# Kernel optimization log

Measured on AMD Instinct MI355X. Metric: run time of the kernel, lower is better.

## Reference

```python
import jax, jax.numpy as jnp
import numpy as np

HIDDEN = 300
LN_EPS = 1e-5


def _pair_indices(L, K):
    # row-major (emo, cau) order matches torch cat/reshape in couple_generator
    i = np.arange(L)[:, None]
    j = np.arange(L)[None, :]
    mask = np.abs(j - i) <= K
    emo, cau = np.nonzero(mask)
    return emo.astype(np.int32), cau.astype(np.int32)


def setup_inputs() -> dict:
    key = jax.random.key(0)
    ks = jax.random.split(key, 10)
    B, L, D = 32, 128, HIDDEN
    K = 12
    pos_dim = 50
    inp = {
        "h_e": jax.random.normal(ks[0], (B, L, D), jnp.float32),
        "h_c": jax.random.normal(ks[1], (B, L, D), jnp.float32),
        "h_share": jax.random.normal(ks[2], (B, L, D), jnp.float32),
        "pos_emb": jax.random.normal(ks[3], (2 * K + 1, pos_dim), jnp.float32) * 0.1,
        "W_hid": jax.random.normal(ks[4], (D, 2 * D + pos_dim), jnp.float32) * 0.02,
        "b_hid": jnp.zeros((D,), jnp.float32),
        "ln_g": jnp.ones((D,), jnp.float32),
        "ln_b": jnp.zeros((D,), jnp.float32),
        "W_rel": jax.random.normal(ks[5], (1, D), jnp.float32) * 0.02,
        "b_rel": jnp.zeros((1,), jnp.float32),
        "K": K,
    }
    return inp


def reference(h_e, h_c, h_share, pos_emb, W_hid, b_hid, ln_g, ln_b, W_rel, b_rel, K):
    B, L, D = h_e.shape
    he = h_e + h_share
    hc = h_c + h_share
    emo, cau = _pair_indices(L, int(K))  # static index constants
    rel = (cau - emo).astype(np.float32)  # [n]
    rp = jnp.asarray(cau - emo + int(K), jnp.int32)  # shifted rel pos
    # gather-concat pair features: [B, n, 2D]
    couples = jnp.concatenate([he[:, emo, :], hc[:, cau, :]], axis=-1)
    # Gaussian kernel over relative positions: [n, n]
    rel_j = jnp.asarray(rel)
    kernel = jnp.exp(-jnp.square(rel_j[:, None] - rel_j[None, :]))
    # smooth position embeddings (batch-independent): [n, pos_dim]
    rel_pos_emb = kernel @ pos_emb[rp]
    pair = jnp.concatenate(
        [couples, jnp.broadcast_to(rel_pos_emb[None], (B,) + rel_pos_emb.shape)],
        axis=-1,
    )
    h = jnp.einsum("bnf,df->bnd", pair, W_hid) + b_hid
    mu = jnp.mean(h, axis=-1, keepdims=True)
    var = jnp.mean(jnp.square(h - mu), axis=-1, keepdims=True)
    h = (h - mu) * jax.lax.rsqrt(var + LN_EPS) * ln_g + ln_b
    h = jax.nn.elu(h)  # dropout is identity in eval mode
    out = jnp.einsum("bnd,od->bno", h, W_rel) + b_rel
    return out[..., 0]  # [B, n_couple]
```

## Files before the change

kernel.cpp:

```cpp
#include <hip/hip_runtime.h>
#include <math.h>

#define BB 32
#define LL 128
#define DD 300
#define PD 50
#define KW 12
#define NP 3044
#define FF 650
#define NR 25
#define KP 320
#define MM 4096
#define LN_EPS 1e-5f

typedef __attribute__((ext_vector_type(8))) short short8;
typedef __attribute__((ext_vector_type(4))) float f32x4;
typedef __attribute__((ext_vector_type(4))) int i32x4;

__device__ __forceinline__ unsigned int cvtpk(float lo, float hi) {
    unsigned int r;
    asm("v_cvt_pk_bf16_f32 %0, %1, %2" : "=v"(r) : "v"(lo), "v"(hi));
    return r;
}

__device__ __forceinline__ short8 as_short8(i32x4 v) {
    union { i32x4 i; short8 s; } u; u.i = v; return u.s;
}

__device__ __forceinline__ int row_start(int i) {
    if (i <= 12) return i * 13 + (i * (i - 1)) / 2;
    if (i <= 116) return 222 + 25 * (i - 12);
    int s = i - 116;
    return 2822 + 24 * s - (s * (s - 1)) / 2;
}

struct B8 { float f[8]; };

__global__ __launch_bounds__(512) void fused_kernel(
    const float* __restrict__ h_e, const float* __restrict__ h_c,
    const float* __restrict__ h_share, const float* __restrict__ pos_emb,
    const float* __restrict__ W_hid, const float* __restrict__ b_hid,
    float* __restrict__ E, float* __restrict__ Cc, float* __restrict__ P,
    float* __restrict__ SEp, float* __restrict__ SP)
{
    const int tid = threadIdx.x;

    __shared__ unsigned short Bs[2][160 * 40];

    if (blockIdx.x < NR) {
        __shared__ float sm[PD];
        __shared__ float wsum[8];
        const int r = blockIdx.x;
        if (tid < PD) {
            float acc = 0.f;
            #pragma unroll
            for (int d2 = 0; d2 < NR; d2++) {
                int ad = d2 - KW; if (ad < 0) ad = -ad;
                float cnt = (float)(LL - ad);
                float diff = (float)(r - d2);
                acc += cnt * expf(-diff * diff) * pos_emb[d2 * PD + tid];
            }
            sm[tid] = acc;
        }
        __syncthreads();
        float mine = 0.f;
        if (tid < DD) {
            float a = b_hid[tid];
            const float* w = W_hid + (size_t)tid * FF + 2 * DD;
            #pragma unroll
            for (int k = 0; k < PD; k++) a += sm[k] * w[k];
            P[r * DD + tid] = a;
            mine = a;
        }
        #pragma unroll
        for (int m = 1; m < 64; m <<= 1) mine += __shfl_xor(mine, m, 64);
        if ((tid & 63) == 0) wsum[tid >> 6] = mine;
        __syncthreads();
        if (tid == 0) {
            float s = 0.f;
            #pragma unroll
            for (int w = 0; w < 8; w++) s += wsum[w];
            SP[r] = s;
        }
        return;
    }

    const int gb = blockIdx.x - NR;
    const int sg = (gb & 7) * 32 + (gb >> 3);
    const int m0 = (sg & 63) * 64;
    const int y  = (sg >> 6) & 1;
    const int z  = sg >> 7;
    const int n0 = y * 160;

    const int wid  = tid >> 6;
    const int lane = tid & 63;
    const int wm = wid & 3;
    const int wn = wid >> 1 >> 1;
    const int nn = lane & 15;
    const int q  = lane >> 4;

    const int row = m0 + wm * 16 + nn;
    const float* xr = (z ? h_c : h_e) + (size_t)row * DD;
    const float* sr = h_share + (size_t)row * DD;
    const float* Wsrc = W_hid + z * DD;

    const int n_a = tid >> 2,        c_a = tid & 3;
    const int d_a = n0 + n_a;
    const int n_b = (tid + 512) >> 2;
    const int d_b = n0 + n_b;
    const bool has_b = (tid < 128);

    B8 ra, rb;
    float4 ax0, ax1, as0, as1;

    auto loadB = [&](int k0) {
        const float* pa = Wsrc + (size_t)d_a * FF + k0 + c_a * 8;
        float2 u0 = *(const float2*)(pa);
        float2 u1 = *(const float2*)(pa + 2);
        float2 u2 = *(const float2*)(pa + 4);
        float2 u3 = *(const float2*)(pa + 6);
        ra.f[0] = u0.x; ra.f[1] = u0.y; ra.f[2] = u1.x; ra.f[3] = u1.y;
        ra.f[4] = u2.x; ra.f[5] = u2.y; ra.f[6] = u3.x; ra.f[7] = u3.y;
        if (has_b) {
            if (d_b < DD) {
                const float* pb = Wsrc + (size_t)d_b * FF + k0 + c_a * 8;
                float2 v0 = *(const float2*)(pb);
                float2 v1 = *(const float2*)(pb + 2);
                float2 v2 = *(const float2*)(pb + 4);
                float2 v3 = *(const float2*)(pb + 6);
                rb.f[0] = v0.x; rb.f[1] = v0.y; rb.f[2] = v1.x; rb.f[3] = v1.y;
                rb.f[4] = v2.x; rb.f[5] = v2.y; rb.f[6] = v3.x; rb.f[7] = v3.y;
            } else {
                #pragma unroll
                for (int u = 0; u < 8; u++) rb.f[u] = 0.f;
            }
        }
    };

    auto writeB = [&](int buf) {
        i32x4 w;
        w[0] = cvtpk(ra.f[0], ra.f[1]); w[1] = cvtpk(ra.f[2], ra.f[3]);
        w[2] = cvtpk(ra.f[4], ra.f[5]); w[3] = cvtpk(ra.f[6], ra.f[7]);
        *(i32x4*)&Bs[buf][n_a * 40 + c_a * 8] = w;
        if (has_b) {
            i32x4 v;
            v[0] = cvtpk(rb.f[0], rb.f[1]); v[1] = cvtpk(rb.f[2], rb.f[3]);
            v[2] = cvtpk(rb.f[4], rb.f[5]); v[3] = cvtpk(rb.f[6], rb.f[7]);
            *(i32x4*)&Bs[buf][n_b * 40 + c_a * 8] = v;
        }
    };

    auto loadA = [&](int k0) {
        const int kb = k0 + q * 8;
        if (kb + 7 < DD) {
            ax0 = *(const float4*)&xr[kb];
            ax1 = *(const float4*)&xr[kb + 4];
            as0 = *(const float4*)&sr[kb];
            as1 = *(const float4*)&sr[kb + 4];
        } else {
            float t[8], u[8];
            #pragma unroll
            for (int uu = 0; uu < 8; uu++) {
                int k = kb + uu;
                t[uu] = (k < DD) ? xr[k] : 0.f;
                u[uu] = (k < DD) ? sr[k] : 0.f;
            }
            ax0 = make_float4(t[0], t[1], t[2], t[3]);
            ax1 = make_float4(t[4], t[5], t[6], t[7]);
            as0 = make_float4(u[0], u[1], u[2], u[3]);
            as1 = make_float4(u[4], u[5], u[6], u[7]);
        }
    };

    f32x4 acc[5];
    #pragma unroll
    for (int f = 0; f < 5; f++) acc[f] = (f32x4){0.f, 0.f, 0.f, 0.f};

    loadB(0);
    loadA(0);
    writeB(0);
    __syncthreads();

    #pragma unroll
    for (int k0i = 0; k0i < 10; k0i++) {
        const int cb = k0i & 1;
        const bool more = (k0i < 9);
        const int kn = (k0i + 1) * 32;

        if (more) loadB(kn);

        i32x4 af;
        af[0] = cvtpk(ax0.x + as0.x, ax0.y + as0.y);
        af[1] = cvtpk(ax0.z + as0.z, ax0.w + as0.w);
        af[2] = cvtpk(ax1.x + as1.x, ax1.y + as1.y);
        af[3] = cvtpk(ax1.z + as1.z, ax1.w + as1.w);
        short8 a = as_short8(af);

        if (more) loadA(kn);

        #pragma unroll
        for (int f = 0; f < 5; f++) {
            short8 b = *(const short8*)&Bs[cb][(wn * 80 + f * 16 + nn) * 40 + q * 8];
            acc[f] = __builtin_amdgcn_mfma_f32_16x16x32_bf16(a, b, acc[f], 0, 0, 0);
        }

        if (more) {
            writeB(cb ^ 1);
            __syncthreads();
        }
    }

    const int orow = m0 + wm * 16 + q * 4;
    float rs[4];
    #pragma unroll
    for (int r2 = 0; r2 < 4; r2++) {
        float v = 0.f;
        #pragma unroll
        for (int f = 0; f < 5; f++) v += acc[f][r2];
        #pragma unroll
        for (int m = 1; m < 16; m <<= 1) v += __shfl_xor(v, m, 64);
        rs[r2] = v;
    }
    if (nn == 0) {
        float* slot = SEp + (size_t)(((z * 2 + y) * 2 + wn)) * MM;
        #pragma unroll
        for (int r2 = 0; r2 < 4; r2++) slot[orow + r2] = rs[r2];
    }

    float* O = z ? Cc : E;
    #pragma unroll
    for (int f = 0; f < 5; f++) {
        int col = n0 + wn * 80 + f * 16 + nn;
        if (col < DD) {
            #pragma unroll
            for (int r2 = 0; r2 < 4; r2++)
                O[(size_t)(orow + r2) * DD + col] = acc[f][r2];
        }
    }
}

__global__ __launch_bounds__(320) void pair_kernel(
    const float* __restrict__ E, const float* __restrict__ Cc,
    const float* __restrict__ P, const float* __restrict__ SEp,
    const float* __restrict__ SP, const float* __restrict__ ln_g,
    const float* __restrict__ ln_b, const float* __restrict__ W_rel,
    const float* __restrict__ b_rel, float* __restrict__ out)
{
    const int wid = threadIdx.x >> 6;
    const int lane = threadIdx.x & 63;
    const int slot = (blockIdx.x & 7) * 512 + (blockIdx.x >> 3);
    const int b = slot >> 7;
    const int i = slot & 127;

    const float* e_row = E + (size_t)slot * DD;

    float e[5], g[5], gb[5], wr[5];
    #pragma unroll
    for (int t = 0; t < 5; t++) {
        int d = lane + 64 * t;
        if (d < DD) {
            e[t]  = e_row[d];
            g[t]  = ln_g[d];
            gb[t] = ln_b[d];
            wr[t] = W_rel[d];
        } else {
            e[t] = 0.f; g[t] = 0.f; gb[t] = 0.f; wr[t] = 0.f;
        }
    }
    const float brel = b_rel[0];
    const float SEi = SEp[slot] + SEp[MM + slot] + SEp[2 * MM + slot] + SEp[3 * MM + slot];
    const float* SC = SEp + 4 * MM;

    int jlo = i - KW; if (jlo < 0) jlo = 0;
    int jhi = i + KW; if (jhi > LL - 1) jhi = LL - 1;
    const int base = b * NP + row_start(i);
    const float inv = 1.f / (float)DD;

    for (int j = jlo + wid; j <= jhi; j += 5) {
        const int bj = b * LL + j;
        const int r = j - i + KW;
        const float* c_row = Cc + (size_t)bj * DD;
        const float* p_row = P + r * DD;

        const float sumh = SEi + SC[bj] + SC[MM + bj] + SC[2 * MM + bj]
                         + SC[3 * MM + bj] + SP[r];

        float h[5];
        float ss = 0.f;
        #pragma unroll
        for (int t = 0; t < 5; t++) {
            int d = lane + 64 * t;
            h[t] = 0.f;
            if (d < DD) {
                h[t] = e[t] + c_row[d] + p_row[d];
                ss += h[t] * h[t];
            }
        }
        #pragma unroll
        for (int m = 1; m < 64; m <<= 1) ss += __shfl_xor(ss, m, 64);

        const float mean = sumh * inv;
        float var = ss * inv - mean * mean;
        if (var < 0.f) var = 0.f;
        const float rstd = rsqrtf(var + LN_EPS);

        float acc = 0.f;
        #pragma unroll
        for (int t = 0; t < 5; t++) {
            int d = lane + 64 * t;
            if (d < DD) {
                float yv = (h[t] - mean) * rstd * g[t] + gb[t];
                float el = yv > 0.f ? yv : (__expf(yv) - 1.f);
                acc += el * wr[t];
            }
        }
        #pragma unroll
        for (int m = 1; m < 64; m <<= 1) acc += __shfl_xor(acc, m, 64);

        if (lane == 0) out[base + (j - jlo)] = acc + brel;
    }
}

extern "C" void kernel_launch(void* const* d_in, const int* in_sizes, int n_in,
                              void* d_out, int out_size, void* d_ws, size_t ws_size,
                              hipStream_t stream) {
    const float* h_e     = (const float*)d_in[0];
    const float* h_c     = (const float*)d_in[1];
    const float* h_share = (const float*)d_in[2];
    const float* pos_emb = (const float*)d_in[3];
    const float* W_hid   = (const float*)d_in[4];
    const float* b_hid   = (const float*)d_in[5];
    const float* ln_g    = (const float*)d_in[6];
    const float* ln_b    = (const float*)d_in[7];
    const float* W_rel   = (const float*)d_in[8];
    const float* b_rel   = (const float*)d_in[9];

    float* out = (float*)d_out;

    float* ws  = (float*)d_ws;
    float* E   = ws;
    float* C   = E + (size_t)MM * DD;
    float* P   = C + (size_t)MM * DD;
    float* SEp = P + NR * DD;
    float* SP  = SEp + 8 * MM;

    fused_kernel<<<dim3(NR + 256), dim3(512), 0, stream>>>(
        h_e, h_c, h_share, pos_emb, W_hid, b_hid, E, C, P, SEp, SP);

    pair_kernel<<<dim3(BB * LL), dim3(320), 0, stream>>>(
        E, C, P, SEp, SP, ln_g, ln_b, W_rel, b_rel, out);
}
```

Measured before the change: 128.1 us.

## Compute LayerNorm second moment algebraically via cross-product moments instead of per-pair reduction

The per-pair sum of squares is expanded as ||e||²+||c||²+||p||²+2(e·c+e·p+c·p). A new moments kernel computes these with bf16 MFMA: an E·Cᵀ batch Gram matrix plus E·P and C·P products, and the fused GEMM epilogue now also writes the row sums of squares. The pair kernel then drops its first cross-lane reduction and reads precomputed scalars. The cost is an extra kernel launch, extra workspace traffic, and the cancellation-prone E[x²]-mean² computed from bf16-rounded dot products, which may lose accuracy.

```diff
diff --git a/kernel.cpp b/kernel.cpp
--- a/kernel.cpp
+++ b/kernel.cpp
@@ -34,6 +34,26 @@
     return 2822 + 24 * s - (s * (s - 1)) / 2;
 }
 
+__device__ __forceinline__ void cvt_store8(unsigned short* dst,
+                                           const float* src, int kb) {
+    float f[8];
+    if (kb + 7 < DD) {
+        float2 a0 = *(const float2*)(src + kb);
+        float2 a1 = *(const float2*)(src + kb + 2);
+        float2 a2 = *(const float2*)(src + kb + 4);
+        float2 a3 = *(const float2*)(src + kb + 6);
+        f[0]=a0.x; f[1]=a0.y; f[2]=a1.x; f[3]=a1.y;
+        f[4]=a2.x; f[5]=a2.y; f[6]=a3.x; f[7]=a3.y;
+    } else {
+        #pragma unroll
+        for (int u = 0; u < 8; u++) { int k = kb + u; f[u] = (k < DD) ? src[k] : 0.f; }
+    }
+    i32x4 w;
+    w[0]=cvtpk(f[0],f[1]); w[1]=cvtpk(f[2],f[3]);
+    w[2]=cvtpk(f[4],f[5]); w[3]=cvtpk(f[6],f[7]);
+    *(i32x4*)dst = w;
+}
+
 struct B8 { float f[8]; };
 
 __global__ __launch_bounds__(512) void fused_kernel(
@@ -41,7 +61,7 @@
     const float* __restrict__ h_share, const float* __restrict__ pos_emb,
     const float* __restrict__ W_hid, const float* __restrict__ b_hid,
     float* __restrict__ E, float* __restrict__ Cc, float* __restrict__ P,
-    float* __restrict__ SEp, float* __restrict__ SP)
+    float* __restrict__ SEp, float* __restrict__ SP, float* __restrict__ SP2)
 {
     const int tid = threadIdx.x;
 
@@ -49,7 +69,7 @@
 
     if (blockIdx.x < NR) {
         __shared__ float sm[PD];
-        __shared__ float wsum[8];
+        __shared__ float wsum[8], wsum2[8];
         const int r = blockIdx.x;
         if (tid < PD) {
             float acc = 0.f;
@@ -63,7 +83,7 @@
             sm[tid] = acc;
         }
         __syncthreads();
-        float mine = 0.f;
+        float mine = 0.f, mine2 = 0.f;
         if (tid < DD) {
             float a = b_hid[tid];
             const float* w = W_hid + (size_t)tid * FF + 2 * DD;
@@ -71,16 +91,21 @@
             for (int k = 0; k < PD; k++) a += sm[k] * w[k];
             P[r * DD + tid] = a;
             mine = a;
-        }
-        #pragma unroll
-        for (int m = 1; m < 64; m <<= 1) mine += __shfl_xor(mine, m, 64);
-        if ((tid & 63) == 0) wsum[tid >> 6] = mine;
+            mine2 = a * a;
+        }
+        #pragma unroll
+        for (int m = 1; m < 64; m <<= 1) {
+            mine  += __shfl_xor(mine, m, 64);
+            mine2 += __shfl_xor(mine2, m, 64);
+        }
+        if ((tid & 63) == 0) { wsum[tid >> 6] = mine; wsum2[tid >> 6] = mine2; }
         __syncthreads();
         if (tid == 0) {
-            float s = 0.f;
-            #pragma unroll
-            for (int w = 0; w < 8; w++) s += wsum[w];
+            float s = 0.f, s2 = 0.f;
+            #pragma unroll
+            for (int w = 0; w < 8; w++) { s += wsum[w]; s2 += wsum2[w]; }
             SP[r] = s;
+            SP2[r] = s2;
         }
         return;
     }
@@ -95,7 +120,7 @@
     const int wid  = tid >> 6;
     const int lane = tid & 63;
     const int wm = wid & 3;
-    const int wn = wid >> 1 >> 1;
+    const int wn = wid >> 2;
     const int nn = lane & 15;
     const int q  = lane >> 4;
 
@@ -211,20 +236,27 @@
     }
 
     const int orow = m0 + wm * 16 + q * 4;
-    float rs[4];
+    float rs[4], rq[4];
     #pragma unroll
     for (int r2 = 0; r2 < 4; r2++) {
-        float v = 0.f;
-        #pragma unroll
-        for (int f = 0; f < 5; f++) v += acc[f][r2];
-        #pragma unroll
-        for (int m = 1; m < 16; m <<= 1) v += __shfl_xor(v, m, 64);
-        rs[r2] = v;
+        float v = 0.f, w2 = 0.f;
+        #pragma unroll
+        for (int f = 0; f < 5; f++) { v += acc[f][r2]; w2 += acc[f][r2] * acc[f][r2]; }
+        #pragma unroll
+        for (int m = 1; m < 16; m <<= 1) {
+            v  += __shfl_xor(v, m, 64);
+            w2 += __shfl_xor(w2, m, 64);
+        }
+        rs[r2] = v; rq[r2] = w2;
     }
     if (nn == 0) {
-        float* slot = SEp + (size_t)(((z * 2 + y) * 2 + wn)) * MM;
-        #pragma unroll
-        for (int r2 = 0; r2 < 4; r2++) slot[orow + r2] = rs[r2];
+        float* sb = SEp + ((size_t)z * MM + orow) * 8;
+        const int part = y * 2 + wn;
+        #pragma unroll
+        for (int r2 = 0; r2 < 4; r2++) {
+            sb[r2 * 8 + part]     = rs[r2];
+            sb[r2 * 8 + 4 + part] = rq[r2];
+        }
     }
 
     float* O = z ? Cc : E;
@@ -239,10 +271,117 @@
     }
 }
 
+__global__ __launch_bounds__(256) void moments_kernel(
+    const float* __restrict__ E, const float* __restrict__ Cc,
+    const float* __restrict__ P, float* __restrict__ EC,
+    float* __restrict__ EP, float* __restrict__ CP)
+{
+    const int tid = threadIdx.x;
+    const int wid = tid >> 6;
+    const int lane = tid & 63;
+    const int nn = lane & 15;
+    const int q  = lane >> 4;
+
+    __shared__ unsigned short sbuf[10240];
+
+    if (blockIdx.x < BB) {
+        const int b = blockIdx.x;
+        const float* Eb = E  + (size_t)b * LL * DD;
+        const float* Cb = Cc + (size_t)b * LL * DD;
+        unsigned short* Es = sbuf;
+        unsigned short* Cs = sbuf + 5120;
+
+        f32x4 acc[2][8];
+        #pragma unroll
+        for (int mr = 0; mr < 2; mr++)
+            #pragma unroll
+            for (int f = 0; f < 8; f++) acc[mr][f] = (f32x4){0.f,0.f,0.f,0.f};
+
+        const int m0 = wid * 32;
+
+        for (int k0 = 0; k0 < KP; k0 += 32) {
+            __syncthreads();
+            #pragma unroll
+            for (int it0 = 0; it0 < 2; it0++) {
+                int it = tid + it0 * 256;
+                int rrow = it >> 2, c = it & 3;
+                cvt_store8(&Es[rrow * 40 + c * 8], Eb + rrow * DD, k0 + c * 8);
+                cvt_store8(&Cs[rrow * 40 + c * 8], Cb + rrow * DD, k0 + c * 8);
+            }
+            __syncthreads();
+            #pragma unroll
+            for (int mr = 0; mr < 2; mr++) {
+                short8 a = *(const short8*)&Es[(m0 + mr * 16 + nn) * 40 + q * 8];
+                #pragma unroll
+                for (int f = 0; f < 8; f++) {
+                    short8 bb = *(const short8*)&Cs[(f * 16 + nn) * 40 + q * 8];
+                    acc[mr][f] = __builtin_amdgcn_mfma_f32_16x16x32_bf16(a, bb, acc[mr][f], 0, 0, 0);
+                }
+            }
+        }
+        float* ECb = EC + (size_t)b * LL * LL;
+        #pragma unroll
+        for (int mr = 0; mr < 2; mr++) {
+            const int orow = m0 + mr * 16 + q * 4;
+            #pragma unroll
+            for (int f = 0; f < 8; f++) {
+                const int col = f * 16 + nn;
+                #pragma unroll
+                for (int r2 = 0; r2 < 4; r2++)
+                    ECb[(orow + r2) * LL + col] = acc[mr][f][r2];
+            }
+        }
+    } else {
+        const int idx2 = blockIdx.x - BB;
+        const int which = idx2 >> 6;
+        const int mb = idx2 & 63;
+        const float* X = (which ? Cc : E) + (size_t)mb * 64 * DD;
+        float* O = which ? CP : EP;
+        unsigned short* Xs = sbuf;
+        unsigned short* Ps = sbuf + 2560;
+
+        f32x4 acc[2];
+        acc[0] = (f32x4){0.f,0.f,0.f,0.f};
+        acc[1] = (f32x4){0.f,0.f,0.f,0.f};
+
+        for (int k0 = 0; k0 < KP; k0 += 32) {
+            __syncthreads();
+            { int rrow = tid >> 2, c = tid & 3;
+              cvt_store8(&Xs[rrow * 40 + c * 8], X + rrow * DD, k0 + c * 8); }
+            if (tid < 128) {
+                int rr = tid >> 2, c = tid & 3;
+                if (rr < NR) {
+                    cvt_store8(&Ps[rr * 40 + c * 8], P + rr * DD, k0 + c * 8);
+                } else {
+                    i32x4 zz = (i32x4){0,0,0,0};
+                    *(i32x4*)&Ps[rr * 40 + c * 8] = zz;
+                }
+            }
+            __syncthreads();
+            short8 a = *(const short8*)&Xs[(wid * 16 + nn) * 40 + q * 8];
+            #pragma unroll
+            for (int f = 0; f < 2; f++) {
+                short8 bb = *(const short8*)&Ps[(f * 16 + nn) * 40 + q * 8];
+                acc[f] = __builtin_amdgcn_mfma_f32_16x16x32_bf16(a, bb, acc[f], 0, 0, 0);
+            }
+        }
+        const int orow = mb * 64 + wid * 16 + q * 4;
+        #pragma unroll
+        for (int f = 0; f < 2; f++) {
+            const int col = f * 16 + nn;
+            #pragma unroll
+            for (int r2 = 0; r2 < 4; r2++)
+                O[(size_t)(orow + r2) * 32 + col] = acc[f][r2];
+        }
+    }
+}
+
 __global__ __launch_bounds__(320) void pair_kernel(
     const float* __restrict__ E, const float* __restrict__ Cc,
     const float* __restrict__ P, const float* __restrict__ SEp,
-    const float* __restrict__ SP, const float* __restrict__ ln_g,
+    const float* __restrict__ SP, const float* __restrict__ SP2,
+    const float* __restrict__ EC, const float* __restrict__ EP,
+    const float* __restrict__ CP, const float* __restrict__ ln_g,
     const float* __restrict__ ln_b, const float* __restrict__ W_rel,
     const float* __restrict__ b_rel, float* __restrict__ out)
 {
@@ -268,8 +407,12 @@
         }
     }
     const float brel = b_rel[0];
-    const float SEi = SEp[slot] + SEp[MM + slot] + SEp[2 * MM + slot] + SEp[3 * MM + slot];
-    const float* SC = SEp + 4 * MM;
+    const float4 se4 = *(const float4*)&SEp[(size_t)slot * 8];
+    const float4 sq4 = *(const float4*)&SEp[(size_t)slot * 8 + 4];
+    const float SEi = se4.x + se4.y + se4.z + se4.w;
+    const float SQi = sq4.x + sq4.y + sq4.z + sq4.w;
+    const float* SC8 = SEp + (size_t)MM * 8;
+    const float* ECb = EC + (size_t)b * LL * LL + (size_t)i * LL;
 
     int jlo = i - KW; if (jlo < 0) jlo = 0;
     int jhi = i + KW; if (jhi > LL - 1) jhi = LL - 1;
@@ -282,25 +425,18 @@
         const float* c_row = Cc + (size_t)bj * DD;
         const float* p_row = P + r * DD;
 
-        const float sumh = SEi + SC[bj] + SC[MM + bj] + SC[2 * MM + bj]
-                         + SC[3 * MM + bj] + SP[r];
-
-        float h[5];
-        float ss = 0.f;
-        #pragma unroll
-        for (int t = 0; t < 5; t++) {
-            int d = lane + 64 * t;
-            h[t] = 0.f;
-            if (d < DD) {
-                h[t] = e[t] + c_row[d] + p_row[d];
-                ss += h[t] * h[t];
-            }
-        }
-        #pragma unroll
-        for (int m = 1; m < 64; m <<= 1) ss += __shfl_xor(ss, m, 64);
+        const float4 scv = *(const float4*)&SC8[(size_t)bj * 8];
+        const float4 qcv = *(const float4*)&SC8[(size_t)bj * 8 + 4];
+        const float ec = ECb[j];
+        const float ep = EP[(size_t)slot * 32 + r];
+        const float cp = CP[(size_t)bj * 32 + r];
+
+        const float sumh = SEi + scv.x + scv.y + scv.z + scv.w + SP[r];
+        const float ssq  = SQi + qcv.x + qcv.y + qcv.z + qcv.w + SP2[r]
+                         + 2.f * (ec + ep + cp);
 
         const float mean = sumh * inv;
-        float var = ss * inv - mean * mean;
+        float var = ssq * inv - mean * mean;
         if (var < 0.f) var = 0.f;
         const float rstd = rsqrtf(var + LN_EPS);
 
@@ -309,7 +445,8 @@
         for (int t = 0; t < 5; t++) {
             int d = lane + 64 * t;
             if (d < DD) {
-                float yv = (h[t] - mean) * rstd * g[t] + gb[t];
+                float h = e[t] + c_row[d] + p_row[d];
+                float yv = (h - mean) * rstd * g[t] + gb[t];
                 float el = yv > 0.f ? yv : (__expf(yv) - 1.f);
                 acc += el * wr[t];
             }
@@ -342,11 +479,17 @@
     float* C   = E + (size_t)MM * DD;
     float* P   = C + (size_t)MM * DD;
     float* SEp = P + NR * DD;
-    float* SP  = SEp + 8 * MM;
+    float* SP  = SEp + (size_t)2 * MM * 8;
+    float* SP2 = SP + 32;
+    float* EC  = SP2 + 32;
+    float* EP  = EC + (size_t)BB * LL * LL;
+    float* CP  = EP + (size_t)MM * 32;
 
     fused_kernel<<<dim3(NR + 256), dim3(512), 0, stream>>>(
-        h_e, h_c, h_share, pos_emb, W_hid, b_hid, E, C, P, SEp, SP);
+        h_e, h_c, h_share, pos_emb, W_hid, b_hid, E, C, P, SEp, SP, SP2);
+
+    moments_kernel<<<dim3(160), dim3(256), 0, stream>>>(E, C, P, EC, EP, CP);
 
     pair_kernel<<<dim3(BB * LL), dim3(320), 0, stream>>>(
-        E, C, P, SEp, SP, ln_g, ln_b, W_rel, b_rel, out);
-}
+        E, C, P, SEp, SP, SP2, EC, EP, CP, ln_g, ln_b, W_rel, b_rel, out);
+}
```

After: 149.2 us. 1.16x slower.
